# Kernel tuning notes

Hardware: AMD Instinct MI355X
Metric: run time of the kernel (lower is better)

## Reference

```python
import jax, jax.numpy as jnp
import numpy as np

N_NODES = 100000
N_EDGES = 1600000
IN_DIM = 128
OUT_DIM = 32
NUM_HEADS = 4


def setup_inputs() -> dict:
    key = jax.random.key(0)
    k1, k2, k3, k4, k5, k6 = jax.random.split(key, 6)
    feat = jax.random.normal(k1, (N_NODES, IN_DIM), dtype=jnp.float32)
    # xavier-uniform-ish scales
    fc_w = jax.random.normal(k2, (OUT_DIM * NUM_HEADS, IN_DIM), dtype=jnp.float32) * (1.0 / np.sqrt(IN_DIM))
    attn_src = jax.random.normal(k3, (1, NUM_HEADS, OUT_DIM), dtype=jnp.float32) * 0.1
    attn_dst = jax.random.normal(k4, (1, NUM_HEADS, OUT_DIM), dtype=jnp.float32) * 0.1
    src = jax.random.randint(k5, (N_EDGES,), 0, N_NODES, dtype=jnp.int64)
    dst = jax.random.randint(k6, (N_EDGES,), 0, N_NODES, dtype=jnp.int64)
    return {"feat": feat, "fc_w": fc_w, "attn_src": attn_src, "attn_dst": attn_dst, "src": src, "dst": dst}


def reference(feat, fc_w, attn_src, attn_dst, src, dst):
    N = feat.shape[0]
    # fc: [N, H*D] -> [N, H, D]
    h = (feat @ fc_w.T).reshape(N, NUM_HEADS, OUT_DIM)
    # per-node attention logits [N, H]
    e_src = jnp.sum(h * attn_src, axis=-1)
    e_dst = jnp.sum(h * attn_dst, axis=-1)
    # per-edge logits, LeakyReLU(0.2)  [E, H]
    e = e_src[src] + e_dst[dst]
    e = jnp.where(e > 0, e, 0.2 * e)
    # edge softmax over incoming edges of each dst node
    m = jax.ops.segment_max(e, dst, num_segments=N)          # [N, H], -inf for empty
    a = jnp.exp(e - m[dst])                                  # [E, H]
    s = jax.ops.segment_sum(a, dst, num_segments=N)          # [N, H]
    a = a / jnp.where(s[dst] > 0, s[dst], 1.0)
    # weighted scatter-sum aggregation: u_mul_e + sum
    msg = h[src] * a[:, :, None]                             # [E, H, D]
    out = jax.ops.segment_sum(msg, dst, num_segments=N)      # [N, H, D]
    h_out = out.reshape(N, NUM_HEADS * OUT_DIM)
    # residual: in_dim == out_dim*num_heads -> identity residual
    return h_out + feat
```

## Files before the change

### kernel.cpp

```cpp
#include <hip/hip_runtime.h>

#define HD 128
#define NHEADS 4
#define MBLK 128
#define APITCH 136

#define CHUNK_SHIFT 8
#define CHUNK_NODES 256
#define MAXCH 512
#define CLCAP 4352
#define PT_EDGES 2048
#define EPT 8
#define CAP 48

#define H8_SCALE   15.875f
#define H8_INVSCALE 0.062992126f

typedef __attribute__((ext_vector_type(8))) short bf16x8;
typedef __attribute__((ext_vector_type(4))) float f32x4;

__device__ __forceinline__ unsigned short f2bf(float x) {
    union { float f; unsigned u; } a; a.f = x;
    unsigned r = a.u + 0x7fffu + ((a.u >> 16) & 1u);
    return (unsigned short)(r >> 16);
}

__global__ __launch_bounds__(256) void partition_edges(
    const int* __restrict__ src, const int* __restrict__ dst,
    int* __restrict__ cursor,
    int2* __restrict__ clist,
    int2* __restrict__ spillP, int* __restrict__ nspillP,
    int E, int nchunks, int spillPCap)
{
    __shared__ int lcnt[MAXCH];
    __shared__ int gbase[MAXCH];
    __shared__ unsigned short rnk[PT_EDGES];
    const int tid = threadIdx.x;
    for (int i = tid; i < MAXCH; i += 256) lcnt[i] = 0;
    __syncthreads();

    const int ebase = blockIdx.x * PT_EDGES;

#pragma unroll
    for (int k = 0; k < EPT; k++) {
        int idx = tid + k * 256;
        int e = ebase + idx;
        if (e < E) {
            int d = dst[e];
            rnk[idx] = (unsigned short)atomicAdd(&lcnt[d >> CHUNK_SHIFT], 1);
        }
    }
    __syncthreads();

    for (int c = tid; c < nchunks; c += 256) {
        int cnt = lcnt[c];
        gbase[c] = cnt ? atomicAdd(&cursor[c], cnt) : 0;
    }
    __syncthreads();

#pragma unroll
    for (int k = 0; k < EPT; k++) {
        int idx = tid + k * 256;
        int e = ebase + idx;
        if (e < E) {
            int d = dst[e], s = src[e];
            int c = d >> CHUNK_SHIFT;
            int pos = gbase[c] + (int)rnk[idx];
            if (pos < CLCAP) {
                clist[(size_t)c * CLCAP + pos] = make_int2(d, s);
            } else {
                int kk = atomicAdd(nspillP, 1);
                if (kk < spillPCap) spillP[kk] = make_int2(d, s);
            }
        }
    }
}

__global__ __launch_bounds__(512) void bucketize(
    const int2* __restrict__ clist, const int* __restrict__ cursor,
    const int2* __restrict__ spillP, const int* __restrict__ nspillP,
    int* __restrict__ erec, int* __restrict__ counts,
    int2* __restrict__ spillB, int* __restrict__ nspillB,
    int N, int spillPCap, int spillBCap)
{
    __shared__ int lcnt[CHUNK_NODES];
    const int c = blockIdx.x;
    const int tid = threadIdx.x;
    if (tid < CHUNK_NODES) lcnt[tid] = 0;
    __syncthreads();

    int cnt = cursor[c]; if (cnt > CLCAP) cnt = CLCAP;
    const int2* base = clist + (size_t)c * CLCAP;
    const int nodebase = c << CHUNK_SHIFT;

    for (int i0 = tid; i0 < cnt; i0 += 512 * 4) {
        int2 p[4]; int pos[4];
#pragma unroll
        for (int k = 0; k < 4; k++) {
            int i = i0 + k * 512;
            p[k] = (i < cnt) ? base[i] : make_int2(nodebase, 0);
        }
#pragma unroll
        for (int k = 0; k < 4; k++) {
            int i = i0 + k * 512;
            pos[k] = (i < cnt) ? atomicAdd(&lcnt[p[k].x - nodebase], 1) : CAP;
        }
#pragma unroll
        for (int k = 0; k < 4; k++) {
            int i = i0 + k * 512;
            if (i < cnt) {
                if (pos[k] < CAP) erec[(size_t)p[k].x * CAP + pos[k]] = p[k].y;
                else { int kk = atomicAdd(nspillB, 1); if (kk < spillBCap) spillB[kk] = p[k]; }
            }
        }
    }
    int nsp = *nspillP; if (nsp > spillPCap) nsp = spillPCap;
    for (int i = tid; i < nsp; i += 512) {
        int2 p = spillP[i];
        if ((p.x >> CHUNK_SHIFT) == c) {
            int pos = atomicAdd(&lcnt[p.x - nodebase], 1);
            if (pos < CAP) erec[(size_t)p.x * CAP + pos] = p.y;
            else { int kk = atomicAdd(nspillB, 1); if (kk < spillBCap) spillB[kk] = p; }
        }
    }
    __syncthreads();
    if (tid < CHUNK_NODES) {
        int n = nodebase + tid;
        if (n < N) counts[n] = lcnt[tid];
    }
}

__global__ __launch_bounds__(256, 2) void gemm_mfma(
    const float* __restrict__ feat, const float* __restrict__ fc_w,
    const float* __restrict__ attn_src, const float* __restrict__ attn_dst,
    signed char* __restrict__ h8, float* __restrict__ e_src, float* __restrict__ e_dst,
    int N)
{
    __shared__ unsigned short As[MBLK * APITCH];
    __shared__ unsigned short Bs[HD * APITCH];
    const int tid = threadIdx.x;
    const int row0 = blockIdx.x * MBLK;

    for (int i = tid; i < 128 * 32; i += 256) {
        int o = i >> 5, j = i & 31;
        float4 v = ((const float4*)fc_w)[i];
        ushort4 u; u.x = f2bf(v.x); u.y = f2bf(v.y); u.z = f2bf(v.z); u.w = f2bf(v.w);
        *(ushort4*)&Bs[o * APITCH + j * 4] = u;
    }
    for (int i = tid; i < MBLK * 32; i += 256) {
        int r = i >> 5, j = i & 31;
        int rowg = row0 + r;
        float4 v = make_float4(0.f, 0.f, 0.f, 0.f);
        if (rowg < N) {
            v = ((const float4*)feat)[(size_t)rowg * 32 + j];
        }
        ushort4 u; u.x = f2bf(v.x); u.y = f2bf(v.y); u.z = f2bf(v.z); u.w = f2bf(v.w);
        *(ushort4*)&As[r * APITCH + j * 4] = u;
    }
    __syncthreads();

    const int w = tid >> 6, lane = tid & 63, quad = lane >> 4, lr = lane & 15;
    f32x4 acc[2][8];
#pragma unroll
    for (int rt = 0; rt < 2; rt++)
#pragma unroll
        for (int ct = 0; ct < 8; ct++) acc[rt][ct] = (f32x4){0.f, 0.f, 0.f, 0.f};

#pragma unroll
    for (int ks = 0; ks < 4; ks++) {
        const int k0 = ks * 32 + quad * 8;
        bf16x8 a0 = *(const bf16x8*)&As[(w * 32 + lr) * APITCH + k0];
        bf16x8 a1 = *(const bf16x8*)&As[(w * 32 + 16 + lr) * APITCH + k0];
        bf16x8 bf[8];
#pragma unroll
        for (int ct = 0; ct < 8; ct++)
            bf[ct] = *(const bf16x8*)&Bs[(ct * 16 + lr) * APITCH + k0];
#pragma unroll
        for (int ct = 0; ct < 8; ct++) {
            acc[0][ct] = __builtin_amdgcn_mfma_f32_16x16x32_bf16(a0, bf[ct], acc[0][ct], 0, 0, 0);
            acc[1][ct] = __builtin_amdgcn_mfma_f32_16x16x32_bf16(a1, bf[ct], acc[1][ct], 0, 0, 0);
        }
    }

#pragma unroll
    for (int rt = 0; rt < 2; rt++) {
#pragma unroll
        for (int ct = 0; ct < 8; ct++) {
            int col = ct * 16 + lr;
#pragma unroll
            for (int reg = 0; reg < 4; reg++) {
                int row = row0 + w * 32 + rt * 16 + quad * 4 + reg;
                if (row < N) {
                    float v = acc[rt][ct][reg];
                    v = fminf(fmaxf(v, -8.f), 8.f);
                    int q = (int)rintf(v * H8_SCALE);
                    h8[(size_t)row * 128 + col] = (signed char)q;
                }
            }
        }
    }

    float as_v[8], ad_v[8];
#pragma unroll
    for (int ct = 0; ct < 8; ct++) {
        as_v[ct] = attn_src[ct * 16 + lr];
        ad_v[ct] = attn_dst[ct * 16 + lr];
    }
#pragma unroll
    for (int rt = 0; rt < 2; rt++) {
#pragma unroll
        for (int reg = 0; reg < 4; reg++) {
            int row = row0 + w * 32 + rt * 16 + quad * 4 + reg;
            float ps[4], pd[4];
#pragma unroll
            for (int hd = 0; hd < 4; hd++) {
                ps[hd] = acc[rt][2 * hd][reg] * as_v[2 * hd] + acc[rt][2 * hd + 1][reg] * as_v[2 * hd + 1];
                pd[hd] = acc[rt][2 * hd][reg] * ad_v[2 * hd] + acc[rt][2 * hd + 1][reg] * ad_v[2 * hd + 1];
            }
#pragma unroll
            for (int off = 1; off < 16; off <<= 1) {
#pragma unroll
                for (int hd = 0; hd < 4; hd++) {
                    ps[hd] += __shfl_xor(ps[hd], off);
                    pd[hd] += __shfl_xor(pd[hd], off);
                }
            }
            if (lr == 0 && row < N) {
                *(float4*)&e_src[(size_t)row * 4] = make_float4(ps[0], ps[1], ps[2], ps[3]);
                *(float4*)&e_dst[(size_t)row * 4] = make_float4(pd[0], pd[1], pd[2], pd[3]);
            }
        }
    }
}

__global__ __launch_bounds__(256, 8) void node_agg(
    const int* __restrict__ erec, const int* __restrict__ counts,
    const signed char* __restrict__ h8,
    const float* __restrict__ e_src, const float* __restrict__ e_dst,
    const float* __restrict__ feat, float* __restrict__ out,
    const int2* __restrict__ spillB, const int* __restrict__ nspillB,
    int N, int spillBCap)
{
    const int lane  = threadIdx.x & 63;
    const int grp8  = lane >> 3;
    const int q     = lane & 7;
    const int head  = q >> 1;

    const int wgid   = (blockIdx.x * 256 + threadIdx.x) >> 6;
    const int nwaves = (gridDim.x * 256) >> 6;

    for (int nb0 = wgid * 8; nb0 < N; nb0 += nwaves * 8) {
        const int n = nb0 + grp8;
        const bool active = (n < N);
        const int deg = active ? counts[n] : 0;
        int md = deg;
        md = max(md, __shfl_xor(md, 8));
        md = max(md, __shfl_xor(md, 16));
        md = max(md, __shfl_xor(md, 32));
        if (md == 0) {
            if (active) {
                const float4* f = (const float4*)(feat + (size_t)n * HD) + q * 4;
                float4* o = (float4*)(out + (size_t)n * HD) + q * 4;
#pragma unroll
                for (int k = 0; k < 4; k++) o[k] = f[k];
            }
            continue;
        }
        const float ed = active ? e_dst[(size_t)n * 4 + head] : 0.f;
        const int fdeg = deg < CAP ? deg : CAP;
        const int mdc = md < CAP ? md : CAP;

        f32x4 a0 = (f32x4){0.f, 0.f, 0.f, 0.f};
        f32x4 a1 = (f32x4){0.f, 0.f, 0.f, 0.f};
        f32x4 a2 = (f32x4){0.f, 0.f, 0.f, 0.f};
        f32x4 a3 = (f32x4){0.f, 0.f, 0.f, 0.f};
        float s_l = 0.f;
#pragma unroll 4
        for (int j = 0; j < mdc; ++j) {
            float ev = 0.f; int si = 0;
            if (j < fdeg) {
                si = erec[(size_t)n * CAP + j];
                float v = e_src[(size_t)si * 4 + head] + ed;
                v = v > 0.f ? v : 0.2f * v;
                ev = __expf(v);
            }
            s_l += ev;
            const float evs = ev * H8_INVSCALE;
            uint4 hv = *(const uint4*)&h8[(size_t)si * 128 + q * 16];
            a0.x += evs * (float)(int)(signed char)(hv.x);
            a0.y += evs * (float)(int)(signed char)(hv.x >> 8);
            a0.z += evs * (float)(int)(signed char)(hv.x >> 16);
            a0.w += evs * (float)(int)(signed char)(hv.x >> 24);
            a1.x += evs * (float)(int)(signed char)(hv.y);
            a1.y += evs * (float)(int)(signed char)(hv.y >> 8);
            a1.z += evs * (float)(int)(signed char)(hv.y >> 16);
            a1.w += evs * (float)(int)(signed char)(hv.y >> 24);
            a2.x += evs * (float)(int)(signed char)(hv.z);
            a2.y += evs * (float)(int)(signed char)(hv.z >> 8);
            a2.z += evs * (float)(int)(signed char)(hv.z >> 16);
            a2.w += evs * (float)(int)(signed char)(hv.z >> 24);
            a3.x += evs * (float)(int)(signed char)(hv.w);
            a3.y += evs * (float)(int)(signed char)(hv.w >> 8);
            a3.z += evs * (float)(int)(signed char)(hv.w >> 16);
            a3.w += evs * (float)(int)(signed char)(hv.w >> 24);
        }
        if (__any(deg > CAP)) {
            int ns = *nspillB; if (ns > spillBCap) ns = spillBCap;
            for (int k = 0; k < ns; ++k) {
                int2 p = spillB[k];
                if (active && deg > CAP && p.x == n) {
                    int si = p.y;
                    float v = e_src[(size_t)si * 4 + head] + ed;
                    v = v > 0.f ? v : 0.2f * v;
                    float ev = __expf(v);
                    s_l += ev;
                    const float evs = ev * H8_INVSCALE;
                    uint4 hv = *(const uint4*)&h8[(size_t)si * 128 + q * 16];
                    a0.x += evs * (float)(int)(signed char)(hv.x);
                    a0.y += evs * (float)(int)(signed char)(hv.x >> 8);
                    a0.z += evs * (float)(int)(signed char)(hv.x >> 16);
                    a0.w += evs * (float)(int)(signed char)(hv.x >> 24);
                    a1.x += evs * (float)(int)(signed char)(hv.y);
                    a1.y += evs * (float)(int)(signed char)(hv.y >> 8);
                    a1.z += evs * (float)(int)(signed char)(hv.y >> 16);
                    a1.w += evs * (float)(int)(signed char)(hv.y >> 24);
                    a2.x += evs * (float)(int)(signed char)(hv.z);
                    a2.y += evs * (float)(int)(signed char)(hv.z >> 8);
                    a2.z += evs * (float)(int)(signed char)(hv.z >> 16);
                    a2.w += evs * (float)(int)(signed char)(hv.z >> 24);
                    a3.x += evs * (float)(int)(signed char)(hv.w);
                    a3.y += evs * (float)(int)(signed char)(hv.w >> 8);
                    a3.z += evs * (float)(int)(signed char)(hv.w >> 16);
                    a3.w += evs * (float)(int)(signed char)(hv.w >> 24);
                }
            }
        }
        if (active) {
            const float inv = (deg > 0) ? (1.0f / s_l) : 0.f;
            const float4* f = (const float4*)(feat + (size_t)n * HD) + q * 4;
            float4* o = (float4*)(out + (size_t)n * HD) + q * 4;
            float4 c0 = f[0], c1 = f[1], c2 = f[2], c3 = f[3];
            c0.x += a0.x * inv; c0.y += a0.y * inv; c0.z += a0.z * inv; c0.w += a0.w * inv;
            c1.x += a1.x * inv; c1.y += a1.y * inv; c1.z += a1.z * inv; c1.w += a1.w * inv;
            c2.x += a2.x * inv; c2.y += a2.y * inv; c2.z += a2.z * inv; c2.w += a2.w * inv;
            c3.x += a3.x * inv; c3.y += a3.y * inv; c3.z += a3.z * inv; c3.w += a3.w * inv;
            o[0] = c0; o[1] = c1; o[2] = c2; o[3] = c3;
        }
    }
}

extern "C" void kernel_launch(void* const* d_in, const int* in_sizes, int n_in,
                              void* d_out, int out_size, void* d_ws, size_t ws_size,
                              hipStream_t stream) {
    const float* feat     = (const float*)d_in[0];
    const float* fc_w     = (const float*)d_in[1];
    const float* attn_src = (const float*)d_in[2];
    const float* attn_dst = (const float*)d_in[3];
    const int*   src      = (const int*)d_in[4];
    const int*   dst      = (const int*)d_in[5];
    const int N = in_sizes[0] / HD;
    const int E = in_sizes[4];
    float* out = (float*)d_out;

    const int nchunks = (N + CHUNK_NODES - 1) >> CHUNK_SHIFT;
    const int spillPCap = E / 8;
    const int spillBCap = E / 8;

    signed char* h8 = (signed char*)d_ws;
    float* e_src  = (float*)(h8 + (size_t)N * HD);
    float* e_dst  = e_src + (size_t)N * NHEADS;
    int* erec     = (int*)(e_dst + (size_t)N * NHEADS);
    int* counts   = erec + (size_t)N * CAP;
    int* cursor   = counts + N;
    int* nspillP  = cursor + nchunks;
    int* nspillB  = nspillP + 1;
    int2* clist   = (int2*)(nspillB + 1);
    int2* spillP  = clist + (size_t)nchunks * CLCAP;
    int2* spillB  = spillP + spillPCap;

    const int npart = (E + PT_EDGES - 1) / PT_EDGES;

    hipMemsetAsync(cursor, 0, (size_t)(nchunks + 2) * sizeof(int), stream);
    partition_edges<<<npart, 256, 0, stream>>>(src, dst, cursor, clist, spillP, nspillP,
                                               E, nchunks, spillPCap);
    bucketize<<<nchunks, 512, 0, stream>>>(clist, cursor, spillP, nspillP,
                                           erec, counts, spillB, nspillB,
                                           N, spillPCap, spillBCap);
    gemm_mfma<<<(N + MBLK - 1) / MBLK, 256, 0, stream>>>(feat, fc_w, attn_src, attn_dst,
                                                         h8, e_src, e_dst, N);
    node_agg<<<2048, 256, 0, stream>>>(erec, counts, h8, e_src, e_dst, feat, out,
                                       spillB, nspillB, N, spillBCap);
}
```

Measured before the change: 273.2 us.

## Fuse bucketize into aggregation using per-block LDS neighbor buckets

Drops the separate bucketize kernel and the global erec/counts arrays. Each 512-thread block owns 64 destination nodes. It scans its 256-node chunk's partitioned edge list, bins source indices into shared-memory buckets with LDS atomics, then aggregates straight from those buckets. This removes the scattered global writes and re-reads of the per-node edge table and one kernel launch. In exchange, each chunk's edge list is read four times (once per sub-block) and the spill list is scanned by every block.

```diff
diff --git a/kernel.cpp b/kernel.cpp
--- a/kernel.cpp
+++ b/kernel.cpp
@@ -6,11 +6,12 @@
 #define APITCH 136
 
 #define CHUNK_SHIFT 8
-#define CHUNK_NODES 256
 #define MAXCH 512
 #define CLCAP 4352
 #define PT_EDGES 2048
 #define EPT 8
+#define SUB_SHIFT 6
+#define SUBN 64
 #define CAP 48
 
 #define H8_SCALE   15.875f
@@ -76,60 +77,6 @@
     }
 }
 
-__global__ __launch_bounds__(512) void bucketize(
-    const int2* __restrict__ clist, const int* __restrict__ cursor,
-    const int2* __restrict__ spillP, const int* __restrict__ nspillP,
-    int* __restrict__ erec, int* __restrict__ counts,
-    int2* __restrict__ spillB, int* __restrict__ nspillB,
-    int N, int spillPCap, int spillBCap)
-{
-    __shared__ int lcnt[CHUNK_NODES];
-    const int c = blockIdx.x;
-    const int tid = threadIdx.x;
-    if (tid < CHUNK_NODES) lcnt[tid] = 0;
-    __syncthreads();
-
-    int cnt = cursor[c]; if (cnt > CLCAP) cnt = CLCAP;
-    const int2* base = clist + (size_t)c * CLCAP;
-    const int nodebase = c << CHUNK_SHIFT;
-
-    for (int i0 = tid; i0 < cnt; i0 += 512 * 4) {
-        int2 p[4]; int pos[4];
-#pragma unroll
-        for (int k = 0; k < 4; k++) {
-            int i = i0 + k * 512;
-            p[k] = (i < cnt) ? base[i] : make_int2(nodebase, 0);
-        }
-#pragma unroll
-        for (int k = 0; k < 4; k++) {
-            int i = i0 + k * 512;
-            pos[k] = (i < cnt) ? atomicAdd(&lcnt[p[k].x - nodebase], 1) : CAP;
-        }
-#pragma unroll
-        for (int k = 0; k < 4; k++) {
-            int i = i0 + k * 512;
-            if (i < cnt) {
-                if (pos[k] < CAP) erec[(size_t)p[k].x * CAP + pos[k]] = p[k].y;
-                else { int kk = atomicAdd(nspillB, 1); if (kk < spillBCap) spillB[kk] = p[k]; }
-            }
-        }
-    }
-    int nsp = *nspillP; if (nsp > spillPCap) nsp = spillPCap;
-    for (int i = tid; i < nsp; i += 512) {
-        int2 p = spillP[i];
-        if ((p.x >> CHUNK_SHIFT) == c) {
-            int pos = atomicAdd(&lcnt[p.x - nodebase], 1);
-            if (pos < CAP) erec[(size_t)p.x * CAP + pos] = p.y;
-            else { int kk = atomicAdd(nspillB, 1); if (kk < spillBCap) spillB[kk] = p; }
-        }
-    }
-    __syncthreads();
-    if (tid < CHUNK_NODES) {
-        int n = nodebase + tid;
-        if (n < N) counts[n] = lcnt[tid];
-    }
-}
-
 __global__ __launch_bounds__(256, 2) void gemm_mfma(
     const float* __restrict__ feat, const float* __restrict__ fc_w,
     const float* __restrict__ attn_src, const float* __restrict__ attn_dst,
@@ -233,119 +180,150 @@
     }
 }
 
-__global__ __launch_bounds__(256, 8) void node_agg(
-    const int* __restrict__ erec, const int* __restrict__ counts,
+__global__ __launch_bounds__(512) void agg_chunk(
+    const int2* __restrict__ clist, const int* __restrict__ cursor,
+    const int2* __restrict__ spillP, const int* __restrict__ nspillP,
     const signed char* __restrict__ h8,
     const float* __restrict__ e_src, const float* __restrict__ e_dst,
     const float* __restrict__ feat, float* __restrict__ out,
-    const int2* __restrict__ spillB, const int* __restrict__ nspillB,
-    int N, int spillBCap)
+    int2* __restrict__ spillB, int* __restrict__ nspillB,
+    int N, int spillPCap, int spillBCap)
 {
-    const int lane  = threadIdx.x & 63;
+    __shared__ int bucket[SUBN][CAP];
+    __shared__ int lcnt[SUBN];
+    const int c = blockIdx.x;
+    const int tid = threadIdx.x;
+    const int nodebase = c << SUB_SHIFT;
+
+    if (tid < SUBN) lcnt[tid] = 0;
+    __syncthreads();
+
+    const int chunkC = c >> (CHUNK_SHIFT - SUB_SHIFT);
+    int cnt = cursor[chunkC]; if (cnt > CLCAP) cnt = CLCAP;
+    const int2* base = clist + (size_t)chunkC * CLCAP;
+    for (int i = tid; i < cnt; i += 512) {
+        int2 p = base[i];
+        if ((p.x >> SUB_SHIFT) == c) {
+            int ln = p.x - nodebase;
+            int pos = atomicAdd(&lcnt[ln], 1);
+            if (pos < CAP) bucket[ln][pos] = p.y;
+            else { int kk = atomicAdd(nspillB, 1); if (kk < spillBCap) spillB[kk] = p; }
+        }
+    }
+    int nsp = *nspillP; if (nsp > spillPCap) nsp = spillPCap;
+    for (int i = tid; i < nsp; i += 512) {
+        int2 p = spillP[i];
+        if ((p.x >> SUB_SHIFT) == c) {
+            int ln = p.x - nodebase;
+            int pos = atomicAdd(&lcnt[ln], 1);
+            if (pos < CAP) bucket[ln][pos] = p.y;
+            else { int kk = atomicAdd(nspillB, 1); if (kk < spillBCap) spillB[kk] = p; }
+        }
+    }
+    __syncthreads();
+
+    const int lane  = tid & 63;
+    const int wid   = tid >> 6;
     const int grp8  = lane >> 3;
     const int q     = lane & 7;
     const int head  = q >> 1;
 
-    const int wgid   = (blockIdx.x * 256 + threadIdx.x) >> 6;
-    const int nwaves = (gridDim.x * 256) >> 6;
-
-    for (int nb0 = wgid * 8; nb0 < N; nb0 += nwaves * 8) {
-        const int n = nb0 + grp8;
-        const bool active = (n < N);
-        const int deg = active ? counts[n] : 0;
-        int md = deg;
-        md = max(md, __shfl_xor(md, 8));
-        md = max(md, __shfl_xor(md, 16));
-        md = max(md, __shfl_xor(md, 32));
-        if (md == 0) {
-            if (active) {
-                const float4* f = (const float4*)(feat + (size_t)n * HD) + q * 4;
-                float4* o = (float4*)(out + (size_t)n * HD) + q * 4;
-#pragma unroll
-                for (int k = 0; k < 4; k++) o[k] = f[k];
-            }
-            continue;
-        }
-        const float ed = active ? e_dst[(size_t)n * 4 + head] : 0.f;
-        const int fdeg = deg < CAP ? deg : CAP;
-        const int mdc = md < CAP ? md : CAP;
-
-        f32x4 a0 = (f32x4){0.f, 0.f, 0.f, 0.f};
-        f32x4 a1 = (f32x4){0.f, 0.f, 0.f, 0.f};
-        f32x4 a2 = (f32x4){0.f, 0.f, 0.f, 0.f};
-        f32x4 a3 = (f32x4){0.f, 0.f, 0.f, 0.f};
-        float s_l = 0.f;
+    const int ln = wid * 8 + grp8;
+    const int n = nodebase + ln;
+    const bool active = (n < N);
+    const int deg = active ? lcnt[ln] : 0;
+    int md = deg;
+    md = max(md, __shfl_xor(md, 8));
+    md = max(md, __shfl_xor(md, 16));
+    md = max(md, __shfl_xor(md, 32));
+    if (md == 0) {
+        if (active) {
+            const float4* f = (const float4*)(feat + (size_t)n * HD) + q * 4;
+            float4* o = (float4*)(out + (size_t)n * HD) + q * 4;
+#pragma unroll
+            for (int k = 0; k < 4; k++) o[k] = f[k];
+        }
+        return;
+    }
+    const float ed = active ? e_dst[(size_t)n * 4 + head] : 0.f;
+    const int fdeg = deg < CAP ? deg : CAP;
+    const int mdc = md < CAP ? md : CAP;
+
+    f32x4 a0 = (f32x4){0.f, 0.f, 0.f, 0.f};
+    f32x4 a1 = (f32x4){0.f, 0.f, 0.f, 0.f};
+    f32x4 a2 = (f32x4){0.f, 0.f, 0.f, 0.f};
+    f32x4 a3 = (f32x4){0.f, 0.f, 0.f, 0.f};
+    float s_l = 0.f;
 #pragma unroll 4
-        for (int j = 0; j < mdc; ++j) {
-            float ev = 0.f; int si = 0;
-            if (j < fdeg) {
-                si = erec[(size_t)n * CAP + j];
+    for (int j = 0; j < mdc; ++j) {
+        float ev = 0.f; int si = 0;
+        if (j < fdeg) {
+            si = bucket[ln][j];
+            float v = e_src[(size_t)si * 4 + head] + ed;
+            v = v > 0.f ? v : 0.2f * v;
+            ev = __expf(v);
+        }
+        s_l += ev;
+        const float evs = ev * H8_INVSCALE;
+        uint4 hv = *(const uint4*)&h8[(size_t)si * 128 + q * 16];
+        a0.x += evs * (float)(int)(signed char)(hv.x);
+        a0.y += evs * (float)(int)(signed char)(hv.x >> 8);
+        a0.z += evs * (float)(int)(signed char)(hv.x >> 16);
+        a0.w += evs * (float)(int)(signed char)(hv.x >> 24);
+        a1.x += evs * (float)(int)(signed char)(hv.y);
+        a1.y += evs * (float)(int)(signed char)(hv.y >> 8);
+        a1.z += evs * (float)(int)(signed char)(hv.y >> 16);
+        a1.w += evs * (float)(int)(signed char)(hv.y >> 24);
+        a2.x += evs * (float)(int)(signed char)(hv.z);
+        a2.y += evs * (float)(int)(signed char)(hv.z >> 8);
+        a2.z += evs * (float)(int)(signed char)(hv.z >> 16);
+        a2.w += evs * (float)(int)(signed char)(hv.z >> 24);
+        a3.x += evs * (float)(int)(signed char)(hv.w);
+        a3.y += evs * (float)(int)(signed char)(hv.w >> 8);
+        a3.z += evs * (float)(int)(signed char)(hv.w >> 16);
+        a3.w += evs * (float)(int)(signed char)(hv.w >> 24);
+    }
+    if (__any(deg > CAP)) {
+        int ns = *nspillB; if (ns > spillBCap) ns = spillBCap;
+        for (int k = 0; k < ns; ++k) {
+            int2 p = spillB[k];
+            if (active && deg > CAP && p.x == n) {
+                int si = p.y;
                 float v = e_src[(size_t)si * 4 + head] + ed;
                 v = v > 0.f ? v : 0.2f * v;
-                ev = __expf(v);
-            }
-            s_l += ev;
-            const float evs = ev * H8_INVSCALE;
-            uint4 hv = *(const uint4*)&h8[(size_t)si * 128 + q * 16];
-            a0.x += evs * (float)(int)(signed char)(hv.x);
-            a0.y += evs * (float)(int)(signed char)(hv.x >> 8);
-            a0.z += evs * (float)(int)(signed char)(hv.x >> 16);
-            a0.w += evs * (float)(int)(signed char)(hv.x >> 24);
-            a1.x += evs * (float)(int)(signed char)(hv.y);
-            a1.y += evs * (float)(int)(signed char)(hv.y >> 8);
-            a1.z += evs * (float)(int)(signed char)(hv.y >> 16);
-            a1.w += evs * (float)(int)(signed char)(hv.y >> 24);
-            a2.x += evs * (float)(int)(signed char)(hv.z);
-            a2.y += evs * (float)(int)(signed char)(hv.z >> 8);
-            a2.z += evs * (float)(int)(signed char)(hv.z >> 16);
-            a2.w += evs * (float)(int)(signed char)(hv.z >> 24);
-            a3.x += evs * (float)(int)(signed char)(hv.w);
-            a3.y += evs * (float)(int)(signed char)(hv.w >> 8);
-            a3.z += evs * (float)(int)(signed char)(hv.w >> 16);
-            a3.w += evs * (float)(int)(signed char)(hv.w >> 24);
-        }
-        if (__any(deg > CAP)) {
-            int ns = *nspillB; if (ns > spillBCap) ns = spillBCap;
-            for (int k = 0; k < ns; ++k) {
-                int2 p = spillB[k];
-                if (active && deg > CAP && p.x == n) {
-                    int si = p.y;
-                    float v = e_src[(size_t)si * 4 + head] + ed;
-                    v = v > 0.f ? v : 0.2f * v;
-                    float ev = __expf(v);
-                    s_l += ev;
-                    const float evs = ev * H8_INVSCALE;
-                    uint4 hv = *(const uint4*)&h8[(size_t)si * 128 + q * 16];
-                    a0.x += evs * (float)(int)(signed char)(hv.x);
-                    a0.y += evs * (float)(int)(signed char)(hv.x >> 8);
-                    a0.z += evs * (float)(int)(signed char)(hv.x >> 16);
-                    a0.w += evs * (float)(int)(signed char)(hv.x >> 24);
-                    a1.x += evs * (float)(int)(signed char)(hv.y);
-                    a1.y += evs * (float)(int)(signed char)(hv.y >> 8);
-                    a1.z += evs * (float)(int)(signed char)(hv.y >> 16);
-                    a1.w += evs * (float)(int)(signed char)(hv.y >> 24);
-                    a2.x += evs * (float)(int)(signed char)(hv.z);
-                    a2.y += evs * (float)(int)(signed char)(hv.z >> 8);
-                    a2.z += evs * (float)(int)(signed char)(hv.z >> 16);
-                    a2.w += evs * (float)(int)(signed char)(hv.z >> 24);
-                    a3.x += evs * (float)(int)(signed char)(hv.w);
-                    a3.y += evs * (float)(int)(signed char)(hv.w >> 8);
-                    a3.z += evs * (float)(int)(signed char)(hv.w >> 16);
-                    a3.w += evs * (float)(int)(signed char)(hv.w >> 24);
-                }
-            }
-        }
-        if (active) {
-            const float inv = (deg > 0) ? (1.0f / s_l) : 0.f;
-            const float4* f = (const float4*)(feat + (size_t)n * HD) + q * 4;
-            float4* o = (float4*)(out + (size_t)n * HD) + q * 4;
-            float4 c0 = f[0], c1 = f[1], c2 = f[2], c3 = f[3];
-            c0.x += a0.x * inv; c0.y += a0.y * inv; c0.z += a0.z * inv; c0.w += a0.w * inv;
-            c1.x += a1.x * inv; c1.y += a1.y * inv; c1.z += a1.z * inv; c1.w += a1.w * inv;
-            c2.x += a2.x * inv; c2.y += a2.y * inv; c2.z += a2.z * inv; c2.w += a2.w * inv;
-            c3.x += a3.x * inv; c3.y += a3.y * inv; c3.z += a3.z * inv; c3.w += a3.w * inv;
-            o[0] = c0; o[1] = c1; o[2] = c2; o[3] = c3;
-        }
+                float ev = __expf(v);
+                s_l += ev;
+                const float evs = ev * H8_INVSCALE;
+                uint4 hv = *(const uint4*)&h8[(size_t)si * 128 + q * 16];
+                a0.x += evs * (float)(int)(signed char)(hv.x);
+                a0.y += evs * (float)(int)(signed char)(hv.x >> 8);
+                a0.z += evs * (float)(int)(signed char)(hv.x >> 16);
+                a0.w += evs * (float)(int)(signed char)(hv.x >> 24);
+                a1.x += evs * (float)(int)(signed char)(hv.y);
+                a1.y += evs * (float)(int)(signed char)(hv.y >> 8);
+                a1.z += evs * (float)(int)(signed char)(hv.y >> 16);
+                a1.w += evs * (float)(int)(signed char)(hv.y >> 24);
+                a2.x += evs * (float)(int)(signed char)(hv.z);
+                a2.y += evs * (float)(int)(signed char)(hv.z >> 8);
+                a2.z += evs * (float)(int)(signed char)(hv.z >> 16);
+                a2.w += evs * (float)(int)(signed char)(hv.z >> 24);
+                a3.x += evs * (float)(int)(signed char)(hv.w);
+                a3.y += evs * (float)(int)(signed char)(hv.w >> 8);
+                a3.z += evs * (float)(int)(signed char)(hv.w >> 16);
+                a3.w += evs * (float)(int)(signed char)(hv.w >> 24);
+            }
+        }
+    }
+    if (active) {
+        const float inv = (deg > 0) ? (1.0f / s_l) : 0.f;
+        const float4* f = (const float4*)(feat + (size_t)n * HD) + q * 4;
+        float4* o = (float4*)(out + (size_t)n * HD) + q * 4;
+        float4 c0 = f[0], c1 = f[1], c2 = f[2], c3 = f[3];
+        c0.x += a0.x * inv; c0.y += a0.y * inv; c0.z += a0.z * inv; c0.w += a0.w * inv;
+        c1.x += a1.x * inv; c1.y += a1.y * inv; c1.z += a1.z * inv; c1.w += a1.w * inv;
+        c2.x += a2.x * inv; c2.y += a2.y * inv; c2.z += a2.z * inv; c2.w += a2.w * inv;
+        c3.x += a3.x * inv; c3.y += a3.y * inv; c3.z += a3.z * inv; c3.w += a3.w * inv;
+        o[0] = c0; o[1] = c1; o[2] = c2; o[3] = c3;
     }
 }
 
@@ -362,19 +340,20 @@
     const int E = in_sizes[4];
     float* out = (float*)d_out;
 
-    const int nchunks = (N + CHUNK_NODES - 1) >> CHUNK_SHIFT;
+    const int nchunks = (N + 255) >> CHUNK_SHIFT;
+    const int nsub    = (N + SUBN - 1) >> SUB_SHIFT;
     const int spillPCap = E / 8;
     const int spillBCap = E / 8;
 
     signed char* h8 = (signed char*)d_ws;
     float* e_src  = (float*)(h8 + (size_t)N * HD);
     float* e_dst  = e_src + (size_t)N * NHEADS;
-    int* erec     = (int*)(e_dst + (size_t)N * NHEADS);
-    int* counts   = erec + (size_t)N * CAP;
-    int* cursor   = counts + N;
+    int* cursor   = (int*)(e_dst + (size_t)N * NHEADS);
     int* nspillP  = cursor + nchunks;
     int* nspillB  = nspillP + 1;
-    int2* clist   = (int2*)(nspillB + 1);
+    int hdr = nchunks + 2;
+    hdr = (hdr + 1) & ~1;
+    int2* clist   = (int2*)(cursor + hdr);
     int2* spillP  = clist + (size_t)nchunks * CLCAP;
     int2* spillB  = spillP + spillPCap;
 
@@ -383,11 +362,9 @@
     hipMemsetAsync(cursor, 0, (size_t)(nchunks + 2) * sizeof(int), stream);
     partition_edges<<<npart, 256, 0, stream>>>(src, dst, cursor, clist, spillP, nspillP,
                                                E, nchunks, spillPCap);
-    bucketize<<<nchunks, 512, 0, stream>>>(clist, cursor, spillP, nspillP,
-                                           erec, counts, spillB, nspillB,
-                                           N, spillPCap, spillBCap);
     gemm_mfma<<<(N + MBLK - 1) / MBLK, 256, 0, stream>>>(feat, fc_w, attn_src, attn_dst,
                                                          h8, e_src, e_dst, N);
-    node_agg<<<2048, 256, 0, stream>>>(erec, counts, h8, e_src, e_dst, feat, out,
-                                       spillB, nspillB, N, spillBCap);
-}
+    agg_chunk<<<nsub, 512, 0, stream>>>(clist, cursor, spillP, nspillP,
+                                        h8, e_src, e_dst, feat, out,
+                                        spillB, nspillB, N, spillPCap, spillBCap);
+}
```

After: 245.3 us. -10.2%, faster.
